# Performance work log

Measured on AMD Instinct MI355X. Metric: run time of the kernel, lower is better.

The kernel has to match this reference:

```python
import jax, jax.numpy as jnp
import numpy as np

# Fixed model constants from setParams()
TAU_W, TAU_N, TAU_R = 1.5e6, 6.0e5, 6.0e4
TAU_E, TAU_G, TAU_A = 2.5e4, 1.0e4, 1.0e4
F_W_MAX, F_N_MAX, F_R_MAX = 6.5, 5.0, 5.0
ALPHA_W, ALPHA_N, ALPHA_R = 0.5, 0.175, 0.13
BETA_W, BETA_R = -0.4, -0.9
GAMMA_E, GAMMA_G, GAMMA_A = 5.0, 4.0, 2.0
H_MAX, THETA_W = 1.0, 2.0
TAU_HW, TAU_HS = 3.483e7, 3.06e7
KAPPA = 1.5
A_RK = (0.5, 0.5, 1.0, 1.0)

T, B = 10000, 512


def setup_inputs() -> dict:
    key = jax.random.key(0)
    noise = 0.05 * jax.random.normal(key, (T, B), dtype=jnp.float32)
    return {
        "noise_input": noise,
        "g_RRe": jnp.float32(1.3),
        "g_RWe": jnp.float32(1.6),
        "g_WNi": jnp.float32(-2.0),
        "g_WRi": jnp.float32(-4.0),
        "g_NRi": jnp.float32(-1.3),
        "g_NWi": jnp.float32(-1.68),
    }


def _heaviside(x):
    # smooth heaviside: sigmoid with steepness 5
    return jax.nn.sigmoid(5.0 * x)


def reference(noise_input, g_RRe, g_RWe, g_WNi, g_WRi, g_NRi, g_NWi):
    b = noise_input.shape[1]
    dt = noise_input.dtype
    init = (
        jnp.full((b,), 6.0, dt),    # f_W
        jnp.full((b,), 1e-3, dt),   # f_N
        jnp.full((b,), 1e-3, dt),   # f_R
        jnp.full((b,), 0.9, dt),    # c_WXi
        jnp.full((b,), 1e-3, dt),   # c_NXi
        jnp.full((b,), 1e-3, dt),   # c_RXe
        jnp.full((b,), 0.5, dt),    # h
    )

    def step(state, noise):
        fW0, fN0, fR0, cW0, cN0, cR0, h0 = state
        # RK moment lists; index 0 is the step's initial value
        fW = [fW0]; fN = [fN0]; fR = [fR0]
        cW = [cW0]; cN = [cN0]; cR = [cR0]; hh = [h0]
        for n in range(4):
            a = A_RK[n]
            I_W = g_NWi * cN[n] + g_RWe * cR[n] + noise
            I_N = g_WNi * cW[n] + noise
            I_R = g_WRi * cW[n] + g_NRi * cN[n] + g_RRe * cR[n] + noise
            fW.append(fW[0] + a * (F_W_MAX * 0.5 * (1.0 + jnp.tanh((I_W - BETA_W) / ALPHA_W)) - fW[n]) / TAU_W)
            fN.append(fN[0] + a * (F_N_MAX * 0.5 * (1.0 + jnp.tanh((I_N + KAPPA * hh[n]) / ALPHA_N)) - fN[n]) / TAU_N)
            fR.append(fR[0] + a * (F_R_MAX * 0.5 * (1.0 + jnp.tanh((I_R - BETA_R) / ALPHA_R)) - fR[n]) / TAU_R)
            cW.append(cW[0] + a * (jnp.tanh(fW[n + 1] / GAMMA_E) - cW[n]) / TAU_E)
            cN.append(cN[0] + a * (jnp.tanh(fN[n + 1] / GAMMA_G) - cN[n]) / TAU_G)
            cR.append(cR[0] + a * (jnp.tanh(fR[n + 1] / GAMMA_A) - cR[n]) / TAU_A)
            hh.append(hh[0] + a * ((H_MAX - hh[n]) / TAU_HW * _heaviside(fW[n] - THETA_W)
                                   - hh[n] / TAU_HS * _heaviside(THETA_W - fW[n])))
        comb = lambda v: (-3.0 * v[0] + 2.0 * v[1] + 4.0 * v[2] + 2.0 * v[3] + v[4]) / 6.0
        new_state = tuple(comb(v) for v in (fW, fN, fR, cW, cN, cR, hh))
        return new_state, jnp.stack(new_state)  # [7, B]

    _, traj = jax.lax.scan(step, init, noise_input)
    return traj  # [T, 7, B]
```

## Files before the change

kernel.cpp:

```cpp
#include <hip/hip_runtime.h>

#define T_STEPS 10000
#define BATCH   512

__device__ __forceinline__ float fexp2(float x) {
#if __has_builtin(__builtin_amdgcn_exp2f)
  return __builtin_amdgcn_exp2f(x);
#else
  return exp2f(x);
#endif
}

__device__ __forceinline__ float frcp(float x) {
#if __has_builtin(__builtin_amdgcn_rcpf)
  return __builtin_amdgcn_rcpf(x);
#else
  return 1.0f / x;
#endif
}

#define PIN(x) asm volatile("" : "+v"(x))

template <int CTRL>
__device__ __forceinline__ float qperm(float v) {
  int i = __builtin_bit_cast(int, v);
#if __has_builtin(__builtin_amdgcn_mov_dpp)
  int r = __builtin_amdgcn_mov_dpp(i, CTRL, 0xF, 0xF, true);
#else
  int r = __builtin_amdgcn_ds_swizzle(i, 0x8000 | CTRL);
#endif
  return __builtin_bit_cast(float, r);
}

__global__ __launch_bounds__(64, 1)
void sleep_rk4_kernel(const float* __restrict__ noise,
                      const float* __restrict__ pgRRe,
                      const float* __restrict__ pgRWe,
                      const float* __restrict__ pgWNi,
                      const float* __restrict__ pgWRi,
                      const float* __restrict__ pgNRi,
                      const float* __restrict__ pgNWi,
                      float* __restrict__ out)
{
  __shared__ float shm[16 * 128];

  const int tid  = (int)(blockIdx.x * 64u + threadIdx.x);
  const int b    = tid >> 2;
  const int bl   = b & 15;
  const int role = tid & 3;

  const float g_RRe = *pgRRe, g_RWe = *pgRWe, g_WNi = *pgWNi;
  const float g_WRi = *pgWRi, g_NRi = *pgNRi, g_NWi = *pgNWi;

  const float L2E = 1.4426950408889634f;
  const float LN2 = 0.6931471805599453f;

  float W1, W2, W3, NSC, BB, qa, qb, pa, pb, cs, ia, ib;
  float f0, c0;
  int v0i, v1i;
  bool role03;

  if (role == 0) {
    const float SC = 2.0f * L2E / 0.5f;
    W1 = SC * g_NWi; W2 = SC * g_RWe; W3 = 0.0f; NSC = SC; BB = SC * 0.4f;
    qa = -1.0f / 1.5e6f; qb = 6.5f / 1.5e6f; pa = 0.0f; pb = -6.5f / 1.5e6f;
    cs = 2.0f * L2E / 5.0f; ia = -1.0f / 2.5e4f; ib = 1.0f / 2.5e4f;
    f0 = 6.0f; c0 = 0.9f; v0i = 0; v1i = 3; role03 = true;
  } else if (role == 1) {
    const float SC = 2.0f * L2E / 0.175f;
    W1 = SC * g_WNi; W2 = SC * 1.5f; W3 = 0.0f; NSC = SC; BB = 0.0f;
    qa = -1.0f / 6.0e5f; qb = 5.0f / 6.0e5f; pa = 0.0f; pb = -5.0f / 6.0e5f;
    cs = 2.0f * L2E / 4.0f; ia = -1.0f / 1.0e4f; ib = 1.0f / 1.0e4f;
    f0 = 1.0e-3f; c0 = 1.0e-3f; v0i = 1; v1i = 4; role03 = false;
  } else if (role == 2) {
    const float SC = 2.0f * L2E / 0.13f;
    W1 = SC * g_WRi; W2 = SC * g_NRi; W3 = SC * g_RRe; NSC = SC; BB = SC * 0.9f;
    qa = -1.0f / 6.0e4f; qb = 5.0f / 6.0e4f; pa = 0.0f; pb = -5.0f / 6.0e4f;
    cs = 2.0f * L2E / 2.0f; ia = -1.0f / 1.0e4f; ib = 1.0f / 1.0e4f;
    f0 = 1.0e-3f; c0 = 1.0e-3f; v0i = 2; v1i = 5; role03 = false;
  } else {
    W1 = 0.0f; W2 = -5.0f * L2E; W3 = 0.0f; NSC = 0.0f; BB = 10.0f * L2E;
    qa = -1.0f / 3.06e7f; qb = 0.0f;
    pa = (1.0f / 3.06e7f - 1.0f / 3.483e7f);
    pb = 1.0f / 3.483e7f;
    cs = 0.0f; ia = 0.0f; ib = 0.0f;
    f0 = 0.5f; c0 = 0.0f; v0i = 6; v1i = 7; role03 = true;
  }

  const float AQAh = 0.5f * qa, AQA1 = qa;
  const float AIAh = 0.5f * ia, AIA1 = ia;
  const float IAC  = ia * cs;
  const float TIA  = 2.0f * ia;
  const float R6   = 0.16666666666666666f;

  float vF[4], vG[4];
  auto frun = [&](float f0b, float Gb, float* v) -> float {
    const float Chb = fmaf(0.5f, Gb, f0b), C1b = f0b + Gb;
    float s0 = f0b, acc = -3.0f * f0b;
    s0 = fmaf(AQAh, s0, Chb); v[0] = s0; acc = fmaf(2.0f, s0, acc);
    s0 = fmaf(AQAh, s0, Chb); v[1] = s0; acc = fmaf(4.0f, s0, acc);
    s0 = fmaf(AQA1, s0, C1b); v[2] = s0; acc = fmaf(2.0f, s0, acc);
    s0 = fmaf(AQA1, s0, C1b); v[3] = s0; acc = fmaf(1.0f, s0, acc);
    float q = acc * R6; q = fmaf(fmaf(q, -6.0f, acc), R6, q); return q;
  };
  const float KF = frun(1.0f, 0.0f, vF);
  const float KG = frun(0.0f, 1.0f, vG);

  auto crun = [&](const float* v, float c0b, float e1u, float vd1) -> float {
    const float E1h = IAC * e1u, E11 = 2.0f * IAC * e1u;
    const float Dh = c0b + 0.5f * vd1, D1 = c0b + vd1;
    float s1 = c0b, acc = -3.0f * c0b;
    s1 = fmaf(AIAh, s1, fmaf(E1h, v[0], Dh)); acc = fmaf(2.0f, s1, acc);
    s1 = fmaf(AIAh, s1, fmaf(E1h, v[1], Dh)); acc = fmaf(4.0f, s1, acc);
    s1 = fmaf(AIA1, s1, fmaf(E11, v[2], D1)); acc = fmaf(2.0f, s1, acc);
    s1 = fmaf(AIA1, s1, fmaf(E11, v[3], D1)); acc = fmaf(1.0f, s1, acc);
    float q = acc * R6; q = fmaf(fmaf(q, -6.0f, acc), R6, q); return q;
  };
  float z4[4] = {0.0f, 0.0f, 0.0f, 0.0f};
  const float KC  = crun(z4, 1.0f, 0.0f, 0.0f);
  const float LAf = crun(vF, 0.0f, 1.0f, 0.0f);
  const float LBf = crun(vG, 0.0f, 1.0f, 0.0f);
  const float KW  = crun(z4, 0.0f, 0.0f, 1.0f);

  const float KGi  = 1.0f / KG;
  const float LBfK = LBf * KGi;
  const float qbK  = qb * KG;

  float LAe, LBK, VDK, PK, tLAe, tLBK, tVDK, tPK;
  auto crefresh_compute = [&](float fcur) {
    const float zb = cs * fcur;
    const float ez = fexp2(zb);
    const float sc_ = frcp(1.0f + ez);
    const float t2 = fmaf(sc_, sc_, -sc_);
    const float e1 = LN2 * t2;
    const float vC = fmaf(-e1, zb, sc_);
    const float VD1 = fmaf(TIA, vC, ib);
    tLAe = LAf * e1; tLBK = LBfK * e1; tVDK = KW * VD1;
    tPK = fmaf(pa, fcur, pb) * KG;
  };
  crefresh_compute(f0);
  LAe = tLAe; LBK = tLBK; VDK = tVDK; PK = tPK;

  float dF = 0.0f, dC = 0.0f;
  float Gq0, Gq1, Gq2, Gq3;

  const int offA = v0i * 16 + bl;
  const int offB = v1i * 16 + bl;

  int ldoff[7], goff[7];
  {
    const int L = (int)threadIdx.x;
    const int bb = (int)(blockIdx.x * 16u);
#pragma unroll
    for (int r = 0; r < 7; ++r) {
      const int F  = r * 64 + L;
      const int s_ = F / 28;
      const int u  = F % 28;
      ldoff[r] = s_ * 128 + u * 4;
      goff[r]  = s_ * 3584 + (u >> 2) * 512 + (u & 3) * 4 + bb;
    }
  }
  float* gflush = out;

  float nb0[16], nb1[16];
#pragma unroll
  for (int j = 0; j < 16; ++j) nb0[j] = noise[b + j * BATCH];

  {
    const float pubS = role03 ? f0 : c0;
    const float xAs = qperm<0x01>(c0);
    const float xBs = qperm<0x1E>(pubS);
    const float YB = fmaf(W1, xAs, fmaf(W2, xBs, fmaf(W3, c0, BB)));
    Gq0 = fmaf(PK, frcp(1.0f + fexp2(fmaf(NSC, nb0[0], YB))), qbK);
    Gq1 = fmaf(PK, frcp(1.0f + fexp2(fmaf(NSC, nb0[1], YB))), qbK);
    Gq2 = fmaf(PK, frcp(1.0f + fexp2(fmaf(NSC, nb0[2], YB))), qbK);
    Gq3 = fmaf(PK, frcp(1.0f + fexp2(fmaf(NSC, nb0[3], YB))), qbK);
  }

  auto GROUP = [&](int SJ, float n0, float n1, float n2, float n3) {
    const float pubS = role03 ? f0 : c0;
    const float pubD = role03 ? dF : dC;
    const float xAs = qperm<0x01>(c0);
    const float xBs = qperm<0x1E>(pubS);
    const float xAd = qperm<0x01>(dC);
    const float xBd = qperm<0x1E>(pubD);
    const float f1 = fmaf(KF, f0, Gq0);
    float YB = fmaf(W3, c0, BB);
    float dY = W3 * dC;
    const float c1 = fmaf(KC, c0, fmaf(LAe, f0, fmaf(LBK, Gq0, VDK)));
    YB = fmaf(W2, xBs, YB);
    dY = fmaf(W2, xBd, dY);
    const float f2 = fmaf(KF, f1, Gq1);
    YB = fmaf(W1, xAs, YB);
    dY = fmaf(W1, xAd, dY);
    const float c2 = fmaf(KC, c1, fmaf(LAe, f1, fmaf(LBK, Gq1, VDK)));
    const float y0 = fmaf(NSC, n0, fmaf(4.5f, dY, YB));
    const float y1 = fmaf(NSC, n1, fmaf(5.5f, dY, YB));
    const float f3 = fmaf(KF, f2, Gq2);
    const float y2 = fmaf(NSC, n2, fmaf(6.5f, dY, YB));
    const float y3 = fmaf(NSC, n3, fmaf(7.5f, dY, YB));
    const float c3 = fmaf(KC, c2, fmaf(LAe, f2, fmaf(LBK, Gq2, VDK)));
    const float e0 = fexp2(y0);
    const float e1_ = fexp2(y1);
    const float f4 = fmaf(KF, f3, Gq3);
    const float e2 = fexp2(y2);
    const float e3 = fexp2(y3);
    const float c4 = fmaf(KC, c3, fmaf(LAe, f3, fmaf(LBK, Gq3, VDK)));
    const float r0 = frcp(1.0f + e0);
    const float r1 = frcp(1.0f + e1_);
    const float r2 = frcp(1.0f + e2);
    const float r3 = frcp(1.0f + e3);
    shm[(SJ + 0) * 128 + offA] = f1;  shm[(SJ + 0) * 128 + offB] = c1;
    shm[(SJ + 1) * 128 + offA] = f2;  shm[(SJ + 1) * 128 + offB] = c2;
    shm[(SJ + 2) * 128 + offA] = f3;  shm[(SJ + 2) * 128 + offB] = c3;
    shm[(SJ + 3) * 128 + offA] = f4;  shm[(SJ + 3) * 128 + offB] = c4;
    Gq0 = fmaf(PK, r0, qbK);
    Gq1 = fmaf(PK, r1, qbK);
    Gq2 = fmaf(PK, r2, qbK);
    Gq3 = fmaf(PK, r3, qbK);
    dF = f4 - f3; dC = c4 - c3;
    f0 = f4; c0 = c4;
  };

  int base = 0;

#define TBLOCK(nbC, nbN)                                                      \
  do {                                                                        \
    int tl = base + 16; if (tl > T_STEPS - 16) tl = T_STEPS - 16;             \
    const float* __restrict__ lp = noise + (size_t)tl * BATCH;                \
    _Pragma("unroll")                                                         \
    for (int j = 0; j < 16; ++j) nbN[j] = lp[b + j * BATCH];                  \
    _Pragma("unroll")                                                         \
    for (int j = 0; j < 16; ++j) PIN(nbC[j]);                                 \
    crefresh_compute(f0);                                                     \
    GROUP(0, nbC[4], nbC[5], nbC[6], nbC[7]);                                 \
    LAe = tLAe; LBK = tLBK; VDK = tVDK; PK = tPK;                             \
    GROUP(4, nbC[8], nbC[9], nbC[10], nbC[11]);                               \
    GROUP(8, nbC[12], nbC[13], nbC[14], nbC[15]);                             \
    PIN(nbN[0]); PIN(nbN[1]); PIN(nbN[2]); PIN(nbN[3]);                       \
    GROUP(12, nbN[0], nbN[1], nbN[2], nbN[3]);                                \
    _Pragma("unroll")                                                         \
    for (int r = 0; r < 7; ++r) {                                             \
      const float4 vv = *(const float4*)&shm[ldoff[r]];                       \
      *(float4*)&gflush[goff[r]] = vv;                                        \
    }                                                                         \
    gflush += 16 * 3584;                                                      \
    base += 16;                                                               \
  } while (0)

  for (int kk = 0; kk < 312; ++kk) {
    TBLOCK(nb0, nb1);
    TBLOCK(nb1, nb0);
  }
  TBLOCK(nb0, nb1);
#undef TBLOCK
}

extern "C" void kernel_launch(void* const* d_in, const int* in_sizes, int n_in,
                              void* d_out, int out_size, void* d_ws, size_t ws_size,
                              hipStream_t stream) {
  const float* noise = (const float*)d_in[0];
  const float* gRRe  = (const float*)d_in[1];
  const float* gRWe  = (const float*)d_in[2];
  const float* gWNi  = (const float*)d_in[3];
  const float* gWRi  = (const float*)d_in[4];
  const float* gNRi  = (const float*)d_in[5];
  const float* gNWi  = (const float*)d_in[6];
  float* out = (float*)d_out;

  sleep_rk4_kernel<<<dim3((BATCH * 4) / 64), dim3(64), 0, stream>>>(
      noise, gRRe, gRWe, gWNi, gWRi, gNRi, gNWi, out);
}
```

Baseline: 510.5 us.

## Widen exchange groups from four to eight steps per cross-lane update

Each group of the recurrence now advances eight time steps between cross-lane exchanges instead of four, with the forcing term for the next eight steps extrapolated further ahead from the last state and its difference. This halves the number of lane permutes and serial exchange points per block of sixteen steps, and gives the scheduler more independent exp and rcp work to overlap. The shared-memory slot layout is remapped so each role writes rows by role index, with the global store offsets permuted to match. The trade-off is longer linear extrapolation of the coupling inputs, which may reduce accuracy, plus higher register pressure.

```diff
diff --git a/kernel.cpp b/kernel.cpp
--- a/kernel.cpp
+++ b/kernel.cpp
@@ -57,7 +57,6 @@
 
   float W1, W2, W3, NSC, BB, qa, qb, pa, pb, cs, ia, ib;
   float f0, c0;
-  int v0i, v1i;
   bool role03;
 
   if (role == 0) {
@@ -65,26 +64,26 @@
     W1 = SC * g_NWi; W2 = SC * g_RWe; W3 = 0.0f; NSC = SC; BB = SC * 0.4f;
     qa = -1.0f / 1.5e6f; qb = 6.5f / 1.5e6f; pa = 0.0f; pb = -6.5f / 1.5e6f;
     cs = 2.0f * L2E / 5.0f; ia = -1.0f / 2.5e4f; ib = 1.0f / 2.5e4f;
-    f0 = 6.0f; c0 = 0.9f; v0i = 0; v1i = 3; role03 = true;
+    f0 = 6.0f; c0 = 0.9f; role03 = true;
   } else if (role == 1) {
     const float SC = 2.0f * L2E / 0.175f;
     W1 = SC * g_WNi; W2 = SC * 1.5f; W3 = 0.0f; NSC = SC; BB = 0.0f;
     qa = -1.0f / 6.0e5f; qb = 5.0f / 6.0e5f; pa = 0.0f; pb = -5.0f / 6.0e5f;
     cs = 2.0f * L2E / 4.0f; ia = -1.0f / 1.0e4f; ib = 1.0f / 1.0e4f;
-    f0 = 1.0e-3f; c0 = 1.0e-3f; v0i = 1; v1i = 4; role03 = false;
+    f0 = 1.0e-3f; c0 = 1.0e-3f; role03 = false;
   } else if (role == 2) {
     const float SC = 2.0f * L2E / 0.13f;
     W1 = SC * g_WRi; W2 = SC * g_NRi; W3 = SC * g_RRe; NSC = SC; BB = SC * 0.9f;
     qa = -1.0f / 6.0e4f; qb = 5.0f / 6.0e4f; pa = 0.0f; pb = -5.0f / 6.0e4f;
     cs = 2.0f * L2E / 2.0f; ia = -1.0f / 1.0e4f; ib = 1.0f / 1.0e4f;
-    f0 = 1.0e-3f; c0 = 1.0e-3f; v0i = 2; v1i = 5; role03 = false;
+    f0 = 1.0e-3f; c0 = 1.0e-3f; role03 = false;
   } else {
     W1 = 0.0f; W2 = -5.0f * L2E; W3 = 0.0f; NSC = 0.0f; BB = 10.0f * L2E;
     qa = -1.0f / 3.06e7f; qb = 0.0f;
     pa = (1.0f / 3.06e7f - 1.0f / 3.483e7f);
     pb = 1.0f / 3.483e7f;
     cs = 0.0f; ia = 0.0f; ib = 0.0f;
-    f0 = 0.5f; c0 = 0.0f; v0i = 6; v1i = 7; role03 = true;
+    f0 = 0.5f; c0 = 0.0f; role03 = true;
   }
 
   const float AQAh = 0.5f * qa, AQA1 = qa;
@@ -142,10 +141,10 @@
   LAe = tLAe; LBK = tLBK; VDK = tVDK; PK = tPK;
 
   float dF = 0.0f, dC = 0.0f;
-  float Gq0, Gq1, Gq2, Gq3;
-
-  const int offA = v0i * 16 + bl;
-  const int offB = v1i * 16 + bl;
+  float Gq0, Gq1, Gq2, Gq3, Gq4, Gq5, Gq6, Gq7;
+
+  const int offA = role * 16 + bl;
+  const int offB = (role + 4) * 16 + bl;
 
   int ldoff[7], goff[7];
   {
@@ -156,8 +155,11 @@
       const int F  = r * 64 + L;
       const int s_ = F / 28;
       const int u  = F % 28;
+      const int rg = u >> 2;
+      const int uu = u & 3;
+      const int v  = (rg == 3) ? 6 : ((rg < 3) ? rg : rg - 1);
       ldoff[r] = s_ * 128 + u * 4;
-      goff[r]  = s_ * 3584 + (u >> 2) * 512 + (u & 3) * 4 + bb;
+      goff[r]  = s_ * 3584 + v * 512 + uu * 4 + bb;
     }
   }
   float* gflush = out;
@@ -175,51 +177,84 @@
     Gq1 = fmaf(PK, frcp(1.0f + fexp2(fmaf(NSC, nb0[1], YB))), qbK);
     Gq2 = fmaf(PK, frcp(1.0f + fexp2(fmaf(NSC, nb0[2], YB))), qbK);
     Gq3 = fmaf(PK, frcp(1.0f + fexp2(fmaf(NSC, nb0[3], YB))), qbK);
+    Gq4 = fmaf(PK, frcp(1.0f + fexp2(fmaf(NSC, nb0[4], YB))), qbK);
+    Gq5 = fmaf(PK, frcp(1.0f + fexp2(fmaf(NSC, nb0[5], YB))), qbK);
+    Gq6 = fmaf(PK, frcp(1.0f + fexp2(fmaf(NSC, nb0[6], YB))), qbK);
+    Gq7 = fmaf(PK, frcp(1.0f + fexp2(fmaf(NSC, nb0[7], YB))), qbK);
   }
 
-  auto GROUP = [&](int SJ, float n0, float n1, float n2, float n3) {
+  auto GROUP8 = [&](int SJ, float n0, float n1, float n2, float n3,
+                    float n4, float n5, float n6, float n7) {
     const float pubS = role03 ? f0 : c0;
     const float pubD = role03 ? dF : dC;
     const float xAs = qperm<0x01>(c0);
     const float xBs = qperm<0x1E>(pubS);
     const float xAd = qperm<0x01>(dC);
     const float xBd = qperm<0x1E>(pubD);
-    const float f1 = fmaf(KF, f0, Gq0);
     float YB = fmaf(W3, c0, BB);
     float dY = W3 * dC;
+    const float f1 = fmaf(KF, f0, Gq0);
     const float c1 = fmaf(KC, c0, fmaf(LAe, f0, fmaf(LBK, Gq0, VDK)));
     YB = fmaf(W2, xBs, YB);
     dY = fmaf(W2, xBd, dY);
     const float f2 = fmaf(KF, f1, Gq1);
+    const float c2 = fmaf(KC, c1, fmaf(LAe, f1, fmaf(LBK, Gq1, VDK)));
     YB = fmaf(W1, xAs, YB);
     dY = fmaf(W1, xAd, dY);
-    const float c2 = fmaf(KC, c1, fmaf(LAe, f1, fmaf(LBK, Gq1, VDK)));
-    const float y0 = fmaf(NSC, n0, fmaf(4.5f, dY, YB));
-    const float y1 = fmaf(NSC, n1, fmaf(5.5f, dY, YB));
     const float f3 = fmaf(KF, f2, Gq2);
-    const float y2 = fmaf(NSC, n2, fmaf(6.5f, dY, YB));
-    const float y3 = fmaf(NSC, n3, fmaf(7.5f, dY, YB));
     const float c3 = fmaf(KC, c2, fmaf(LAe, f2, fmaf(LBK, Gq2, VDK)));
+    const float y0 = fmaf(NSC, n0, fmaf( 8.5f, dY, YB));
+    const float y1 = fmaf(NSC, n1, fmaf( 9.5f, dY, YB));
+    const float y2 = fmaf(NSC, n2, fmaf(10.5f, dY, YB));
+    const float y3 = fmaf(NSC, n3, fmaf(11.5f, dY, YB));
+    const float f4 = fmaf(KF, f3, Gq3);
+    const float c4 = fmaf(KC, c3, fmaf(LAe, f3, fmaf(LBK, Gq3, VDK)));
+    const float y4 = fmaf(NSC, n4, fmaf(12.5f, dY, YB));
+    const float y5 = fmaf(NSC, n5, fmaf(13.5f, dY, YB));
+    const float y6 = fmaf(NSC, n6, fmaf(14.5f, dY, YB));
+    const float y7 = fmaf(NSC, n7, fmaf(15.5f, dY, YB));
     const float e0 = fexp2(y0);
     const float e1_ = fexp2(y1);
-    const float f4 = fmaf(KF, f3, Gq3);
+    const float f5 = fmaf(KF, f4, Gq4);
+    const float c5 = fmaf(KC, c4, fmaf(LAe, f4, fmaf(LBK, Gq4, VDK)));
     const float e2 = fexp2(y2);
     const float e3 = fexp2(y3);
-    const float c4 = fmaf(KC, c3, fmaf(LAe, f3, fmaf(LBK, Gq3, VDK)));
+    const float f6 = fmaf(KF, f5, Gq5);
+    const float c6 = fmaf(KC, c5, fmaf(LAe, f5, fmaf(LBK, Gq5, VDK)));
+    const float e4 = fexp2(y4);
+    const float e5 = fexp2(y5);
+    const float f7 = fmaf(KF, f6, Gq6);
+    const float c7 = fmaf(KC, c6, fmaf(LAe, f6, fmaf(LBK, Gq6, VDK)));
+    const float e6 = fexp2(y6);
+    const float e7 = fexp2(y7);
+    const float f8 = fmaf(KF, f7, Gq7);
+    const float c8 = fmaf(KC, c7, fmaf(LAe, f7, fmaf(LBK, Gq7, VDK)));
     const float r0 = frcp(1.0f + e0);
     const float r1 = frcp(1.0f + e1_);
     const float r2 = frcp(1.0f + e2);
     const float r3 = frcp(1.0f + e3);
+    const float r4 = frcp(1.0f + e4);
+    const float r5 = frcp(1.0f + e5);
+    const float r6 = frcp(1.0f + e6);
+    const float r7 = frcp(1.0f + e7);
     shm[(SJ + 0) * 128 + offA] = f1;  shm[(SJ + 0) * 128 + offB] = c1;
     shm[(SJ + 1) * 128 + offA] = f2;  shm[(SJ + 1) * 128 + offB] = c2;
     shm[(SJ + 2) * 128 + offA] = f3;  shm[(SJ + 2) * 128 + offB] = c3;
     shm[(SJ + 3) * 128 + offA] = f4;  shm[(SJ + 3) * 128 + offB] = c4;
+    shm[(SJ + 4) * 128 + offA] = f5;  shm[(SJ + 4) * 128 + offB] = c5;
+    shm[(SJ + 5) * 128 + offA] = f6;  shm[(SJ + 5) * 128 + offB] = c6;
+    shm[(SJ + 6) * 128 + offA] = f7;  shm[(SJ + 6) * 128 + offB] = c7;
+    shm[(SJ + 7) * 128 + offA] = f8;  shm[(SJ + 7) * 128 + offB] = c8;
     Gq0 = fmaf(PK, r0, qbK);
     Gq1 = fmaf(PK, r1, qbK);
     Gq2 = fmaf(PK, r2, qbK);
     Gq3 = fmaf(PK, r3, qbK);
-    dF = f4 - f3; dC = c4 - c3;
-    f0 = f4; c0 = c4;
+    Gq4 = fmaf(PK, r4, qbK);
+    Gq5 = fmaf(PK, r5, qbK);
+    Gq6 = fmaf(PK, r6, qbK);
+    Gq7 = fmaf(PK, r7, qbK);
+    dF = f8 - f7; dC = c8 - c7;
+    f0 = f8; c0 = c8;
   };
 
   int base = 0;
@@ -231,14 +266,15 @@
     _Pragma("unroll")                                                         \
     for (int j = 0; j < 16; ++j) nbN[j] = lp[b + j * BATCH];                  \
     _Pragma("unroll")                                                         \
-    for (int j = 0; j < 16; ++j) PIN(nbC[j]);                                 \
+    for (int j = 8; j < 16; ++j) PIN(nbC[j]);                                 \
     crefresh_compute(f0);                                                     \
-    GROUP(0, nbC[4], nbC[5], nbC[6], nbC[7]);                                 \
+    GROUP8(0, nbC[8], nbC[9], nbC[10], nbC[11],                               \
+              nbC[12], nbC[13], nbC[14], nbC[15]);                            \
     LAe = tLAe; LBK = tLBK; VDK = tVDK; PK = tPK;                             \
-    GROUP(4, nbC[8], nbC[9], nbC[10], nbC[11]);                               \
-    GROUP(8, nbC[12], nbC[13], nbC[14], nbC[15]);                             \
     PIN(nbN[0]); PIN(nbN[1]); PIN(nbN[2]); PIN(nbN[3]);                       \
-    GROUP(12, nbN[0], nbN[1], nbN[2], nbN[3]);                                \
+    PIN(nbN[4]); PIN(nbN[5]); PIN(nbN[6]); PIN(nbN[7]);                       \
+    GROUP8(8, nbN[0], nbN[1], nbN[2], nbN[3],                                 \
+              nbN[4], nbN[5], nbN[6], nbN[7]);                                \
     _Pragma("unroll")                                                         \
     for (int r = 0; r < 7; ++r) {                                             \
       const float4 vv = *(const float4*)&shm[ldoff[r]];                       \
```

Result: faster. 471.9 us (-7.6%).
